# Kernel optimization log

Hardware: AMD Instinct MI355X
Metric: run time of the kernel (lower is better)

The kernel has to match this reference:

```python
import jax, jax.numpy as jnp
import numpy as np

N_NODES = 50000
N_EDGES = 800000
DIM = 64
N_ETYPES = 4
N_STEPS = 5


def setup_inputs() -> dict:
    key = jax.random.key(0)
    ks = jax.random.split(key, 10)
    feat = jax.random.normal(ks[0], (N_NODES, DIM), dtype=jnp.float32)
    src = jax.random.randint(ks[1], (N_EDGES,), 0, N_NODES, dtype=jnp.int32)
    dst = jax.random.randint(ks[2], (N_EDGES,), 0, N_NODES, dtype=jnp.int32)
    etypes = jax.random.randint(ks[3], (N_EDGES,), 0, N_ETYPES, dtype=jnp.int32)
    # per-edge-type Linear weights, xavier_normal with relu gain, zero bias
    gain = float(np.sqrt(2.0))
    std = gain * float(np.sqrt(2.0 / (DIM + DIM)))
    W = jax.random.normal(ks[4], (N_ETYPES, DIM, DIM), dtype=jnp.float32) * std  # [T, out, in]
    b = jnp.zeros((N_ETYPES, DIM), dtype=jnp.float32)
    # GRUCell params (torch layout: [3*dim, dim], gates order r,z,n), uniform(-1/sqrt(dim), 1/sqrt(dim))
    bound = 1.0 / float(np.sqrt(DIM))
    w_ih = jax.random.uniform(ks[5], (3 * DIM, DIM), minval=-bound, maxval=bound, dtype=jnp.float32)
    w_hh = jax.random.uniform(ks[6], (3 * DIM, DIM), minval=-bound, maxval=bound, dtype=jnp.float32)
    b_ih = jax.random.uniform(ks[7], (3 * DIM,), minval=-bound, maxval=bound, dtype=jnp.float32)
    b_hh = jax.random.uniform(ks[8], (3 * DIM,), minval=-bound, maxval=bound, dtype=jnp.float32)
    return {"feat": feat, "W": W, "b": b, "w_ih": w_ih, "w_hh": w_hh,
            "b_ih": b_ih, "b_hh": b_hh, "src": src, "dst": dst, "etypes": etypes}


def _gru_cell(a, h, w_ih, w_hh, b_ih, b_hh):
    gi = a @ w_ih.T + b_ih  # [N, 3*D]
    gh = h @ w_hh.T + b_hh
    i_r, i_z, i_n = jnp.split(gi, 3, axis=-1)
    h_r, h_z, h_n = jnp.split(gh, 3, axis=-1)
    r = jax.nn.sigmoid(i_r + h_r)
    z = jax.nn.sigmoid(i_z + h_z)
    n = jnp.tanh(i_n + r * h_n)
    return (1.0 - z) * n + z * h


def reference(feat, W, b, w_ih, w_hh, b_ih, b_hh, src, dst, etypes):
    n_nodes = feat.shape[0]
    h = feat
    for _ in range(N_STEPS):
        # apply every etype linear to all nodes: [N, T, D]
        h_all = jnp.einsum('nd,ted->nte', h, W) + b
        # per-edge message selects src node under its edge type: [E, D]
        m = h_all[src, etypes]
        # scatter-sum to destination nodes: [N, D]
        a = jax.ops.segment_sum(m, dst, num_segments=n_nodes)
        h = _gru_cell(a, h, w_ih, w_hh, b_ih, b_hh)
    return h
```

## Files before the change

### kernel.cpp

```cpp
#include <hip/hip_runtime.h>
#include <hip/hip_bf16.h>
#include <cstdint>

#define DIM 64
#define TD 256
#define NSTEPS 5
#define HS  68
#define GLDH 194
#define MAXDEG 64

typedef __attribute__((ext_vector_type(8))) short short8v;
typedef __attribute__((ext_vector_type(4))) float f32x4;
typedef __attribute__((ext_vector_type(8))) _Float16 half8v;

__device__ __forceinline__ float sigmoidf_(float x){ return 1.0f/(1.0f+expf(-x)); }

__device__ __forceinline__ unsigned short f2bf(float x){
  unsigned u = __builtin_bit_cast(unsigned, x);
  return (unsigned short)((u + 0x7FFFu + ((u>>16)&1u)) >> 16);
}
__device__ __forceinline__ float bf2f(unsigned short b){
  unsigned u = ((unsigned)b)<<16;
  return __builtin_bit_cast(float, u);
}

__device__ __forceinline__ void splitbf8(const float* __restrict__ p,
                                         short8v& hi, short8v& lo){
  float4 x0 = *(const float4*)p;
  float4 x1 = *(const float4*)(p+4);
  float xs[8] = {x0.x,x0.y,x0.z,x0.w,x1.x,x1.y,x1.z,x1.w};
#pragma unroll
  for(int i=0;i<8;i++){
    unsigned short hb = f2bf(xs[i]);
    float rem = xs[i] - bf2f(hb);
    hi[i] = (short)hb;
    lo[i] = (short)f2bf(rem);
  }
}

__global__ __launch_bounds__(256) void k_pack(const float* __restrict__ src,
    short* __restrict__ ph, short* __restrict__ pl, int ncoltiles, int mode){
  int idx = blockIdx.x*256 + threadIdx.x;
  int total = ncoltiles*1024;
  if (idx >= total) return;
  int e = idx & 7, lane = (idx>>3)&63, kc = (idx>>9)&1, ct = idx>>10;
  int col = ct*16 + (lane&15);
  int k = kc*32 + (lane>>4)*8 + e;
  float v;
  if (mode==0){ int t = col>>6, eo = col&63; v = src[(size_t)(t*64+eo)*64 + k]; }
  else        { v = src[(size_t)col*64 + k]; }
  unsigned short hb = f2bf(v);
  float rem = v - bf2f(hb);
  ph[idx] = (short)hb;
  pl[idx] = (short)f2bf(rem);
}

__global__ __launch_bounds__(256) void k_transform_mfma(
    const float* __restrict__ h, const short* __restrict__ pth,
    const short* __restrict__ ptl, const float* __restrict__ b,
    _Float16* __restrict__ h_all, int n_nodes){
  const int wave = threadIdx.x >> 6, lane = threadIdx.x & 63;
  const int n0 = blockIdx.x * 16;
  if (n0 >= n_nodes) return;
  const int arow = n0 + (lane & 15);
  const int kb = (lane >> 4) * 8;
  short8v ah0,al0,ah1,al1;
  splitbf8(h + (size_t)arow*DIM + kb,      ah0, al0);
  splitbf8(h + (size_t)arow*DIM + 32 + kb, ah1, al1);
  const int crow = n0 + (lane >> 4) * 4;
  const int cc = lane & 15;
#pragma unroll
  for (int i = 0; i < 4; ++i){
    int ct = wave*4 + i;
    const short8v bh0 = *(const short8v*)(pth + ((size_t)(ct*2+0)*64 + lane)*8);
    const short8v bh1 = *(const short8v*)(pth + ((size_t)(ct*2+1)*64 + lane)*8);
    const short8v bl0 = *(const short8v*)(ptl + ((size_t)(ct*2+0)*64 + lane)*8);
    const short8v bl1 = *(const short8v*)(ptl + ((size_t)(ct*2+1)*64 + lane)*8);
    float bias = b[ct*16 + cc];
    f32x4 acc = {bias,bias,bias,bias};
    acc = __builtin_amdgcn_mfma_f32_16x16x32_bf16(ah0, bh0, acc, 0,0,0);
    acc = __builtin_amdgcn_mfma_f32_16x16x32_bf16(ah1, bh1, acc, 0,0,0);
    acc = __builtin_amdgcn_mfma_f32_16x16x32_bf16(al0, bh0, acc, 0,0,0);
    acc = __builtin_amdgcn_mfma_f32_16x16x32_bf16(al1, bh1, acc, 0,0,0);
    acc = __builtin_amdgcn_mfma_f32_16x16x32_bf16(ah0, bl0, acc, 0,0,0);
    acc = __builtin_amdgcn_mfma_f32_16x16x32_bf16(ah1, bl1, acc, 0,0,0);
#pragma unroll
    for (int q=0;q<4;q++)
      h_all[(size_t)(crow + q)*TD + ct*16 + cc] = (_Float16)acc[q];
  }
}

__global__ __launch_bounds__(256) void k_scatter_ell(
    const int* __restrict__ src, const int* __restrict__ dst,
    const int* __restrict__ et, int* __restrict__ deg,
    int* __restrict__ ell, int n_edges) {
  int e = blockIdx.x * 256 + threadIdx.x;
  if (e >= n_edges) return;
  int d0 = dst[e];
  int rank = atomicAdd(&deg[d0], 1);
  if (rank < MAXDEG)
    ell[(size_t)d0 * MAXDEG + rank] = (src[e] << 2) | et[e];
}

__global__ __launch_bounds__(256) void k_step(
    const _Float16* __restrict__ h_in, _Float16* __restrict__ h_out,
    const int* __restrict__ ell, const int* __restrict__ deg,
    float* __restrict__ h,
    const short* __restrict__ pih_h, const short* __restrict__ pih_l,
    const short* __restrict__ phh_h, const short* __restrict__ phh_l,
    const float* __restrict__ b_ih, const float* __restrict__ b_hh,
    const short* __restrict__ pth, const short* __restrict__ ptl,
    const float* __restrict__ bb,
    int n_nodes, int do_transform){
  __shared__ __align__(16) char smem[4352 + 12416];
  float (*atile)[HS]      = (float(*)[HS])smem;
  float (*hnew)[HS]       = (float(*)[HS])smem;
  int   (*ells)[MAXDEG]   = (int(*)[MAXDEG])(smem + 4352);
  _Float16* gbuf          = (_Float16*)(smem + 4352);

  const int tid = threadIdx.x;
  const int wave = tid >> 6, lane = tid & 63;
  const int n0 = blockIdx.x * 16;
  if (n0 >= n_nodes) return;

  {
    int j = tid >> 4, c4 = (tid & 15) * 4;
    int4 v = *(const int4*)(ell + (size_t)(n0 + j) * MAXDEG + c4);
    *(int4*)&ells[j][c4] = v;
  }
  __syncthreads();

  {
    int j = tid >> 4;
    int q = tid & 15;
    int eslot = q >> 3;
    int dimg = q & 7;
    int node = n0 + j;
    int dg = min(deg[node], MAXDEG);
    float acc[8] = {0,0,0,0,0,0,0,0};
    int i = eslot;
    for (; i + 6 < dg; i += 8) {
      int p0 = ells[j][i], p1 = ells[j][i+2], p2 = ells[j][i+4], p3 = ells[j][i+6];
      half8v v0 = *(const half8v*)(h_in + (size_t)(p0>>2)*TD + (p0&3)*DIM + dimg*8);
      half8v v1 = *(const half8v*)(h_in + (size_t)(p1>>2)*TD + (p1&3)*DIM + dimg*8);
      half8v v2 = *(const half8v*)(h_in + (size_t)(p2>>2)*TD + (p2&3)*DIM + dimg*8);
      half8v v3 = *(const half8v*)(h_in + (size_t)(p3>>2)*TD + (p3&3)*DIM + dimg*8);
#pragma unroll
      for (int k=0;k<8;k++)
        acc[k] += ((float)v0[k] + (float)v1[k]) + ((float)v2[k] + (float)v3[k]);
    }
    for (; i < dg; i += 2) {
      int p0 = ells[j][i];
      half8v v0 = *(const half8v*)(h_in + (size_t)(p0>>2)*TD + (p0&3)*DIM + dimg*8);
#pragma unroll
      for (int k=0;k<8;k++) acc[k] += (float)v0[k];
    }
#pragma unroll
    for (int k=0;k<8;k++) acc[k] += __shfl_xor(acc[k], 8);
    if (eslot == 0) {
#pragma unroll
      for (int k=0;k<8;k++) atile[j][dimg*8+k] = acc[k];
    }
  }
  __syncthreads();

  const bool is_h = wave >= 2;
  const short* __restrict__ pbh = is_h ? phh_h : pih_h;
  const short* __restrict__ pbl = is_h ? phh_l : pih_l;
  const float* __restrict__ bv  = is_h ? b_hh : b_ih;
  _Float16* outb = gbuf + (is_h ? 16*GLDH : 0);

  const int kb = (lane >> 4) * 8;
  short8v ah0,al0,ah1,al1;
  if (is_h) {
    const float* xp = h + (size_t)(n0 + (lane & 15))*DIM;
    splitbf8(xp + kb,      ah0, al0);
    splitbf8(xp + 32 + kb, ah1, al1);
  } else {
    const float* xp = &atile[lane & 15][0];
    splitbf8(xp + kb,      ah0, al0);
    splitbf8(xp + 32 + kb, ah1, al1);
  }

  const int ct0 = (wave & 1) * 6;
  const int rr = (lane >> 4) * 4;
  const int cc = lane & 15;
#pragma unroll
  for (int i = 0; i < 6; ++i){
    int ct = ct0 + i;
    const short8v bh0 = *(const short8v*)(pbh + ((size_t)(ct*2+0)*64 + lane)*8);
    const short8v bh1 = *(const short8v*)(pbh + ((size_t)(ct*2+1)*64 + lane)*8);
    const short8v bl0 = *(const short8v*)(pbl + ((size_t)(ct*2+0)*64 + lane)*8);
    const short8v bl1 = *(const short8v*)(pbl + ((size_t)(ct*2+1)*64 + lane)*8);
    float bias = bv[ct*16 + cc];
    f32x4 acc = {bias,bias,bias,bias};
    acc = __builtin_amdgcn_mfma_f32_16x16x32_bf16(ah0, bh0, acc, 0,0,0);
    acc = __builtin_amdgcn_mfma_f32_16x16x32_bf16(ah1, bh1, acc, 0,0,0);
    acc = __builtin_amdgcn_mfma_f32_16x16x32_bf16(al0, bh0, acc, 0,0,0);
    acc = __builtin_amdgcn_mfma_f32_16x16x32_bf16(al1, bh1, acc, 0,0,0);
    acc = __builtin_amdgcn_mfma_f32_16x16x32_bf16(ah0, bl0, acc, 0,0,0);
    acc = __builtin_amdgcn_mfma_f32_16x16x32_bf16(ah1, bl1, acc, 0,0,0);
#pragma unroll
    for (int q=0;q<4;q++)
      outb[(rr+q)*GLDH + ct*16 + cc] = (_Float16)acc[q];
  }
  __syncthreads();

#pragma unroll
  for (int it=0; it<4; ++it){
    int t = it*256 + tid;
    int j = t >> 6, d = t & 63;
    float gir = (float)gbuf[j*GLDH + d];
    float giz = (float)gbuf[j*GLDH + 64 + d];
    float gin = (float)gbuf[j*GLDH + 128 + d];
    float ghr = (float)gbuf[16*GLDH + j*GLDH + d];
    float ghz = (float)gbuf[16*GLDH + j*GLDH + 64 + d];
    float ghn = (float)gbuf[16*GLDH + j*GLDH + 128 + d];
    float r  = sigmoidf_(gir + ghr);
    float z  = sigmoidf_(giz + ghz);
    float nv = tanhf    (gin + r*ghn);
    size_t off = (size_t)(n0+j)*DIM + d;
    float ho = h[off];
    float hn = (1.0f - z)*nv + z*ho;
    h[off] = hn;
    hnew[j][d] = hn;
  }
  if (!do_transform) return;
  __syncthreads();

  short8v th0,tl0,th1,tl1;
  splitbf8(&hnew[lane & 15][kb],      th0, tl0);
  splitbf8(&hnew[lane & 15][32 + kb], th1, tl1);
  const int crow = n0 + (lane >> 4) * 4;
#pragma unroll
  for (int i = 0; i < 4; ++i){
    int ct = wave*4 + i;
    const short8v bh0 = *(const short8v*)(pth + ((size_t)(ct*2+0)*64 + lane)*8);
    const short8v bh1 = *(const short8v*)(pth + ((size_t)(ct*2+1)*64 + lane)*8);
    const short8v bl0 = *(const short8v*)(ptl + ((size_t)(ct*2+0)*64 + lane)*8);
    const short8v bl1 = *(const short8v*)(ptl + ((size_t)(ct*2+1)*64 + lane)*8);
    float bias = bb[ct*16 + cc];
    f32x4 acc = {bias,bias,bias,bias};
    acc = __builtin_amdgcn_mfma_f32_16x16x32_bf16(th0, bh0, acc, 0,0,0);
    acc = __builtin_amdgcn_mfma_f32_16x16x32_bf16(th1, bh1, acc, 0,0,0);
    acc = __builtin_amdgcn_mfma_f32_16x16x32_bf16(tl0, bh0, acc, 0,0,0);
    acc = __builtin_amdgcn_mfma_f32_16x16x32_bf16(tl1, bh1, acc, 0,0,0);
    acc = __builtin_amdgcn_mfma_f32_16x16x32_bf16(th0, bl0, acc, 0,0,0);
    acc = __builtin_amdgcn_mfma_f32_16x16x32_bf16(th1, bl1, acc, 0,0,0);
#pragma unroll
    for (int q=0;q<4;q++)
      h_out[(size_t)(crow + q)*TD + ct*16 + cc] = (_Float16)acc[q];
  }
}

extern "C" void kernel_launch(void* const* d_in, const int* in_sizes, int n_in,
                              void* d_out, int out_size, void* d_ws, size_t ws_size,
                              hipStream_t stream) {
  const float* feat = (const float*)d_in[0];
  const float* W    = (const float*)d_in[1];
  const float* b    = (const float*)d_in[2];
  const float* w_ih = (const float*)d_in[3];
  const float* w_hh = (const float*)d_in[4];
  const float* b_ih = (const float*)d_in[5];
  const float* b_hh = (const float*)d_in[6];
  const int* src = (const int*)d_in[7];
  const int* dst = (const int*)d_in[8];
  const int* et  = (const int*)d_in[9];

  const int n_nodes = in_sizes[0] / DIM;
  const int n_edges = in_sizes[7];

  float* h = (float*)d_out;
  char* ws = (char*)d_ws;
  _Float16* hall0 = (_Float16*)ws;  ws += (size_t)n_nodes * TD * sizeof(_Float16);
  _Float16* hall1 = (_Float16*)ws;  ws += (size_t)n_nodes * TD * sizeof(_Float16);
  int* ell     = (int*)ws;      ws += (size_t)n_nodes * MAXDEG * sizeof(int);
  int* deg     = (int*)ws;      ws += (size_t)n_nodes * sizeof(int);
  short* pt_h  = (short*)ws;    ws += 16384 * sizeof(short);
  short* pt_l  = (short*)ws;    ws += 16384 * sizeof(short);
  short* pih_h = (short*)ws;    ws += 12288 * sizeof(short);
  short* pih_l = (short*)ws;    ws += 12288 * sizeof(short);
  short* phh_h = (short*)ws;    ws += 12288 * sizeof(short);
  short* phh_l = (short*)ws;    ws += 12288 * sizeof(short);

  hipMemcpyAsync(h, feat, (size_t)n_nodes * DIM * sizeof(float),
                 hipMemcpyDeviceToDevice, stream);

  k_pack<<<64, 256, 0, stream>>>(W,    pt_h,  pt_l,  16, 0);
  k_pack<<<48, 256, 0, stream>>>(w_ih, pih_h, pih_l, 12, 1);
  k_pack<<<48, 256, 0, stream>>>(w_hh, phh_h, phh_l, 12, 1);

  const int nblk_edges = (n_edges + 255) / 256;
  hipMemsetAsync(deg, 0, (size_t)n_nodes * sizeof(int), stream);
  k_scatter_ell<<<nblk_edges, 256, 0, stream>>>(src, dst, et, deg, ell, n_edges);

  const int rtiles = (n_nodes + 15) / 16;

  k_transform_mfma<<<rtiles, 256, 0, stream>>>(h, pt_h, pt_l, b, hall0, n_nodes);
  for (int s = 0; s < NSTEPS; ++s) {
    const _Float16* hin = (s & 1) ? hall1 : hall0;
    _Float16* hout      = (s & 1) ? hall0 : hall1;
    k_step<<<rtiles, 256, 0, stream>>>(hin, hout, ell, deg, h,
                                       pih_h, pih_l, phh_h, phh_l, b_ih, b_hh,
                                       pt_h, pt_l, b, n_nodes,
                                       (s < NSTEPS - 1) ? 1 : 0);
  }
}
```

Baseline: 308.8 us.

## Aggregate raw features per (dst,etype) then apply edge-type linear after scatter

Replaces the transform-then-gather scheme with gather-then-transform. Edges are bucketed by (destination, edge type) into a virtual ELL, raw fp16 node features (64 wide instead of 256) are summed per bucket, and a K=288 MFMA applies all four type weights plus degree-scaled bias in one pass. This cuts the gathered bytes per edge by four and removes the separate transform kernel and 256-wide intermediate buffer. In exchange there is a larger per-block MFMA, a bigger ELL (4x32 slots per node, with a tighter cap per type), and fp16 rounding of h before aggregation.

```diff
diff --git a/kernel.cpp b/kernel.cpp
--- a/kernel.cpp
+++ b/kernel.cpp
@@ -3,11 +3,11 @@
 #include <cstdint>
 
 #define DIM 64
-#define TD 256
 #define NSTEPS 5
 #define HS  68
 #define GLDH 194
-#define MAXDEG 64
+#define ATS 292
+#define MAXVDEG 32
 
 typedef __attribute__((ext_vector_type(8))) short short8v;
 typedef __attribute__((ext_vector_type(4))) float f32x4;
@@ -39,84 +39,69 @@
 }
 
 __global__ __launch_bounds__(256) void k_pack(const float* __restrict__ src,
-    short* __restrict__ ph, short* __restrict__ pl, int ncoltiles, int mode){
+    short* __restrict__ ph, short* __restrict__ pl, int ncoltiles){
   int idx = blockIdx.x*256 + threadIdx.x;
   int total = ncoltiles*1024;
   if (idx >= total) return;
   int e = idx & 7, lane = (idx>>3)&63, kc = (idx>>9)&1, ct = idx>>10;
   int col = ct*16 + (lane&15);
   int k = kc*32 + (lane>>4)*8 + e;
-  float v;
-  if (mode==0){ int t = col>>6, eo = col&63; v = src[(size_t)(t*64+eo)*64 + k]; }
-  else        { v = src[(size_t)col*64 + k]; }
+  float v = src[(size_t)col*DIM + k];
   unsigned short hb = f2bf(v);
-  float rem = v - bf2f(hb);
   ph[idx] = (short)hb;
-  pl[idx] = (short)f2bf(rem);
-}
-
-__global__ __launch_bounds__(256) void k_transform_mfma(
-    const float* __restrict__ h, const short* __restrict__ pth,
-    const short* __restrict__ ptl, const float* __restrict__ b,
-    _Float16* __restrict__ h_all, int n_nodes){
-  const int wave = threadIdx.x >> 6, lane = threadIdx.x & 63;
-  const int n0 = blockIdx.x * 16;
-  if (n0 >= n_nodes) return;
-  const int arow = n0 + (lane & 15);
-  const int kb = (lane >> 4) * 8;
-  short8v ah0,al0,ah1,al1;
-  splitbf8(h + (size_t)arow*DIM + kb,      ah0, al0);
-  splitbf8(h + (size_t)arow*DIM + 32 + kb, ah1, al1);
-  const int crow = n0 + (lane >> 4) * 4;
-  const int cc = lane & 15;
-#pragma unroll
-  for (int i = 0; i < 4; ++i){
-    int ct = wave*4 + i;
-    const short8v bh0 = *(const short8v*)(pth + ((size_t)(ct*2+0)*64 + lane)*8);
-    const short8v bh1 = *(const short8v*)(pth + ((size_t)(ct*2+1)*64 + lane)*8);
-    const short8v bl0 = *(const short8v*)(ptl + ((size_t)(ct*2+0)*64 + lane)*8);
-    const short8v bl1 = *(const short8v*)(ptl + ((size_t)(ct*2+1)*64 + lane)*8);
-    float bias = b[ct*16 + cc];
-    f32x4 acc = {bias,bias,bias,bias};
-    acc = __builtin_amdgcn_mfma_f32_16x16x32_bf16(ah0, bh0, acc, 0,0,0);
-    acc = __builtin_amdgcn_mfma_f32_16x16x32_bf16(ah1, bh1, acc, 0,0,0);
-    acc = __builtin_amdgcn_mfma_f32_16x16x32_bf16(al0, bh0, acc, 0,0,0);
-    acc = __builtin_amdgcn_mfma_f32_16x16x32_bf16(al1, bh1, acc, 0,0,0);
-    acc = __builtin_amdgcn_mfma_f32_16x16x32_bf16(ah0, bl0, acc, 0,0,0);
-    acc = __builtin_amdgcn_mfma_f32_16x16x32_bf16(ah1, bl1, acc, 0,0,0);
-#pragma unroll
-    for (int q=0;q<4;q++)
-      h_all[(size_t)(crow + q)*TD + ct*16 + cc] = (_Float16)acc[q];
-  }
-}
-
-__global__ __launch_bounds__(256) void k_scatter_ell(
+  pl[idx] = (short)f2bf(v - bf2f(hb));
+}
+
+__global__ __launch_bounds__(256) void k_pack256(const float* __restrict__ W,
+    const float* __restrict__ b, short* __restrict__ ph, short* __restrict__ pl){
+  int idx = blockIdx.x*256 + threadIdx.x;
+  if (idx >= 4*9*512) return;
+  int e = idx & 7, lane = (idx>>3)&63, r = idx>>9;
+  int kc = r % 9, ct = r / 9;
+  int col = ct*16 + (lane&15);
+  int k = kc*32 + (lane>>4)*8 + e;
+  float v = 0.0f;
+  if (k < 256){ int t = k>>6, d = k&63; v = W[(size_t)(t*64+col)*DIM + d]; }
+  else if (k < 260){ v = b[(size_t)(k-256)*DIM + col]; }
+  unsigned short hb = f2bf(v);
+  ph[idx] = (short)hb;
+  pl[idx] = (short)f2bf(v - bf2f(hb));
+}
+
+__global__ __launch_bounds__(256) void k_cast(const float* __restrict__ x,
+                                              _Float16* __restrict__ y, int n4){
+  int i = blockIdx.x*256 + threadIdx.x;
+  if (i >= n4) return;
+  float4 v = *(const float4*)(x + (size_t)i*4);
+  y[(size_t)i*4+0] = (_Float16)v.x; y[(size_t)i*4+1] = (_Float16)v.y;
+  y[(size_t)i*4+2] = (_Float16)v.z; y[(size_t)i*4+3] = (_Float16)v.w;
+}
+
+__global__ __launch_bounds__(256) void k_scatter_vell(
     const int* __restrict__ src, const int* __restrict__ dst,
-    const int* __restrict__ et, int* __restrict__ deg,
+    const int* __restrict__ et, int* __restrict__ deg4,
     int* __restrict__ ell, int n_edges) {
   int e = blockIdx.x * 256 + threadIdx.x;
   if (e >= n_edges) return;
-  int d0 = dst[e];
-  int rank = atomicAdd(&deg[d0], 1);
-  if (rank < MAXDEG)
-    ell[(size_t)d0 * MAXDEG + rank] = (src[e] << 2) | et[e];
+  int vn = dst[e]*4 + et[e];
+  int rank = atomicAdd(&deg4[vn], 1);
+  if (rank < MAXVDEG)
+    ell[(size_t)vn * MAXVDEG + rank] = src[e];
 }
 
 __global__ __launch_bounds__(256) void k_step(
-    const _Float16* __restrict__ h_in, _Float16* __restrict__ h_out,
-    const int* __restrict__ ell, const int* __restrict__ deg,
+    const _Float16* __restrict__ hb_in, _Float16* __restrict__ hb_out,
+    const int* __restrict__ ell, const int* __restrict__ deg4,
     float* __restrict__ h,
+    const short* __restrict__ pw_h, const short* __restrict__ pw_l,
     const short* __restrict__ pih_h, const short* __restrict__ pih_l,
     const short* __restrict__ phh_h, const short* __restrict__ phh_l,
     const float* __restrict__ b_ih, const float* __restrict__ b_hh,
-    const short* __restrict__ pth, const short* __restrict__ ptl,
-    const float* __restrict__ bb,
-    int n_nodes, int do_transform){
-  __shared__ __align__(16) char smem[4352 + 12416];
-  float (*atile)[HS]      = (float(*)[HS])smem;
-  float (*hnew)[HS]       = (float(*)[HS])smem;
-  int   (*ells)[MAXDEG]   = (int(*)[MAXDEG])(smem + 4352);
-  _Float16* gbuf          = (_Float16*)(smem + 4352);
+    int n_nodes, int write_hb){
+  __shared__ __align__(16) char smem[16*ATS*4 + 16*HS*4];
+  float (*atile)[ATS] = (float(*)[ATS])smem;
+  _Float16* gbuf      = (_Float16*)smem;
+  float (*abuf)[HS]   = (float(*)[HS])(smem + 16*ATS*4);
 
   const int tid = threadIdx.x;
   const int wave = tid >> 6, lane = tid & 63;
@@ -124,43 +109,66 @@
   if (n0 >= n_nodes) return;
 
   {
-    int j = tid >> 4, c4 = (tid & 15) * 4;
-    int4 v = *(const int4*)(ell + (size_t)(n0 + j) * MAXDEG + c4);
-    *(int4*)&ells[j][c4] = v;
+    int vl = tid >> 2;
+    int q  = tid & 3;
+    int jn = vl >> 2;
+    int t  = vl & 3;
+    int vng = (n0 << 2) + vl;
+    int dg = min(deg4[vng], MAXVDEG);
+    const int* ebase = ell + (size_t)vng * MAXVDEG;
+    float acc[16];
+#pragma unroll
+    for (int k=0;k<16;k++) acc[k]=0.0f;
+    int i = 0;
+    for (; i + 1 < dg; i += 2) {
+      int s0 = ebase[i], s1 = ebase[i+1];
+      half8v a0 = *(const half8v*)(hb_in + (size_t)s0*DIM + q*16);
+      half8v a1 = *(const half8v*)(hb_in + (size_t)s0*DIM + q*16 + 8);
+      half8v c0 = *(const half8v*)(hb_in + (size_t)s1*DIM + q*16);
+      half8v c1 = *(const half8v*)(hb_in + (size_t)s1*DIM + q*16 + 8);
+#pragma unroll
+      for (int k=0;k<8;k++){ acc[k]   += (float)a0[k] + (float)c0[k];
+                             acc[8+k] += (float)a1[k] + (float)c1[k]; }
+    }
+    if (i < dg) {
+      int s0 = ebase[i];
+      half8v a0 = *(const half8v*)(hb_in + (size_t)s0*DIM + q*16);
+      half8v a1 = *(const half8v*)(hb_in + (size_t)s0*DIM + q*16 + 8);
+#pragma unroll
+      for (int k=0;k<8;k++){ acc[k] += (float)a0[k]; acc[8+k] += (float)a1[k]; }
+    }
+    float* dstp = &atile[jn][t*64 + q*16];
+#pragma unroll
+    for (int w=0;w<4;w++){
+      float4 v = {acc[w*4+0],acc[w*4+1],acc[w*4+2],acc[w*4+3]};
+      *(float4*)(dstp + w*4) = v;
+    }
+    if (q == 0) atile[jn][256 + t] = (float)dg;
+    int zr = tid >> 4, zc = 260 + (tid & 15);
+    atile[zr][zc] = 0.0f;
+    atile[zr][zc + 16] = 0.0f;
   }
   __syncthreads();
 
+  const int rr = (lane >> 4) * 4;
+  const int cc = lane & 15;
   {
-    int j = tid >> 4;
-    int q = tid & 15;
-    int eslot = q >> 3;
-    int dimg = q & 7;
-    int node = n0 + j;
-    int dg = min(deg[node], MAXDEG);
-    float acc[8] = {0,0,0,0,0,0,0,0};
-    int i = eslot;
-    for (; i + 6 < dg; i += 8) {
-      int p0 = ells[j][i], p1 = ells[j][i+2], p2 = ells[j][i+4], p3 = ells[j][i+6];
-      half8v v0 = *(const half8v*)(h_in + (size_t)(p0>>2)*TD + (p0&3)*DIM + dimg*8);
-      half8v v1 = *(const half8v*)(h_in + (size_t)(p1>>2)*TD + (p1&3)*DIM + dimg*8);
-      half8v v2 = *(const half8v*)(h_in + (size_t)(p2>>2)*TD + (p2&3)*DIM + dimg*8);
-      half8v v3 = *(const half8v*)(h_in + (size_t)(p3>>2)*TD + (p3&3)*DIM + dimg*8);
-#pragma unroll
-      for (int k=0;k<8;k++)
-        acc[k] += ((float)v0[k] + (float)v1[k]) + ((float)v2[k] + (float)v3[k]);
-    }
-    for (; i < dg; i += 2) {
-      int p0 = ells[j][i];
-      half8v v0 = *(const half8v*)(h_in + (size_t)(p0>>2)*TD + (p0&3)*DIM + dimg*8);
-#pragma unroll
-      for (int k=0;k<8;k++) acc[k] += (float)v0[k];
-    }
-#pragma unroll
-    for (int k=0;k<8;k++) acc[k] += __shfl_xor(acc[k], 8);
-    if (eslot == 0) {
-#pragma unroll
-      for (int k=0;k<8;k++) atile[j][dimg*8+k] = acc[k];
-    }
+    const float* arow = &atile[lane & 15][0];
+    const int koff = (lane >> 4) * 8;
+    f32x4 acc4 = {0.f,0.f,0.f,0.f};
+#pragma unroll
+    for (int kc = 0; kc < 9; ++kc){
+      short8v ah, al;
+      splitbf8(arow + kc*32 + koff, ah, al);
+      const short8v bh = *(const short8v*)(pw_h + ((size_t)(wave*9+kc)*64 + lane)*8);
+      const short8v bl = *(const short8v*)(pw_l + ((size_t)(wave*9+kc)*64 + lane)*8);
+      acc4 = __builtin_amdgcn_mfma_f32_16x16x32_bf16(ah, bl, acc4, 0,0,0);
+      acc4 = __builtin_amdgcn_mfma_f32_16x16x32_bf16(al, bh, acc4, 0,0,0);
+      acc4 = __builtin_amdgcn_mfma_f32_16x16x32_bf16(ah, bh, acc4, 0,0,0);
+    }
+    __syncthreads();
+#pragma unroll
+    for (int q=0;q<4;q++) abuf[rr+q][wave*16 + cc] = acc4[q];
   }
   __syncthreads();
 
@@ -177,14 +185,12 @@
     splitbf8(xp + kb,      ah0, al0);
     splitbf8(xp + 32 + kb, ah1, al1);
   } else {
-    const float* xp = &atile[lane & 15][0];
+    const float* xp = &abuf[lane & 15][0];
     splitbf8(xp + kb,      ah0, al0);
     splitbf8(xp + 32 + kb, ah1, al1);
   }
 
   const int ct0 = (wave & 1) * 6;
-  const int rr = (lane >> 4) * 4;
-  const int cc = lane & 15;
 #pragma unroll
   for (int i = 0; i < 6; ++i){
     int ct = ct0 + i;
@@ -223,33 +229,7 @@
     float ho = h[off];
     float hn = (1.0f - z)*nv + z*ho;
     h[off] = hn;
-    hnew[j][d] = hn;
-  }
-  if (!do_transform) return;
-  __syncthreads();
-
-  short8v th0,tl0,th1,tl1;
-  splitbf8(&hnew[lane & 15][kb],      th0, tl0);
-  splitbf8(&hnew[lane & 15][32 + kb], th1, tl1);
-  const int crow = n0 + (lane >> 4) * 4;
-#pragma unroll
-  for (int i = 0; i < 4; ++i){
-    int ct = wave*4 + i;
-    const short8v bh0 = *(const short8v*)(pth + ((size_t)(ct*2+0)*64 + lane)*8);
-    const short8v bh1 = *(const short8v*)(pth + ((size_t)(ct*2+1)*64 + lane)*8);
-    const short8v bl0 = *(const short8v*)(ptl + ((size_t)(ct*2+0)*64 + lane)*8);
-    const short8v bl1 = *(const short8v*)(ptl + ((size_t)(ct*2+1)*64 + lane)*8);
-    float bias = bb[ct*16 + cc];
-    f32x4 acc = {bias,bias,bias,bias};
-    acc = __builtin_amdgcn_mfma_f32_16x16x32_bf16(th0, bh0, acc, 0,0,0);
-    acc = __builtin_amdgcn_mfma_f32_16x16x32_bf16(th1, bh1, acc, 0,0,0);
-    acc = __builtin_amdgcn_mfma_f32_16x16x32_bf16(tl0, bh0, acc, 0,0,0);
-    acc = __builtin_amdgcn_mfma_f32_16x16x32_bf16(tl1, bh1, acc, 0,0,0);
-    acc = __builtin_amdgcn_mfma_f32_16x16x32_bf16(th0, bl0, acc, 0,0,0);
-    acc = __builtin_amdgcn_mfma_f32_16x16x32_bf16(th1, bl1, acc, 0,0,0);
-#pragma unroll
-    for (int q=0;q<4;q++)
-      h_out[(size_t)(crow + q)*TD + ct*16 + cc] = (_Float16)acc[q];
+    if (write_hb) hb_out[off] = (_Float16)hn;
   }
 }
 
@@ -272,37 +252,37 @@
 
   float* h = (float*)d_out;
   char* ws = (char*)d_ws;
-  _Float16* hall0 = (_Float16*)ws;  ws += (size_t)n_nodes * TD * sizeof(_Float16);
-  _Float16* hall1 = (_Float16*)ws;  ws += (size_t)n_nodes * TD * sizeof(_Float16);
-  int* ell     = (int*)ws;      ws += (size_t)n_nodes * MAXDEG * sizeof(int);
-  int* deg     = (int*)ws;      ws += (size_t)n_nodes * sizeof(int);
-  short* pt_h  = (short*)ws;    ws += 16384 * sizeof(short);
-  short* pt_l  = (short*)ws;    ws += 16384 * sizeof(short);
-  short* pih_h = (short*)ws;    ws += 12288 * sizeof(short);
-  short* pih_l = (short*)ws;    ws += 12288 * sizeof(short);
-  short* phh_h = (short*)ws;    ws += 12288 * sizeof(short);
-  short* phh_l = (short*)ws;    ws += 12288 * sizeof(short);
+  _Float16* hb0 = (_Float16*)ws;  ws += (size_t)n_nodes * DIM * sizeof(_Float16);
+  _Float16* hb1 = (_Float16*)ws;  ws += (size_t)n_nodes * DIM * sizeof(_Float16);
+  int* ell  = (int*)ws;   ws += (size_t)n_nodes * 4 * MAXVDEG * sizeof(int);
+  int* deg4 = (int*)ws;   ws += (size_t)n_nodes * 4 * sizeof(int);
+  short* pw_h  = (short*)ws;  ws += 18432 * sizeof(short);
+  short* pw_l  = (short*)ws;  ws += 18432 * sizeof(short);
+  short* pih_h = (short*)ws;  ws += 12288 * sizeof(short);
+  short* pih_l = (short*)ws;  ws += 12288 * sizeof(short);
+  short* phh_h = (short*)ws;  ws += 12288 * sizeof(short);
+  short* phh_l = (short*)ws;  ws += 12288 * sizeof(short);
 
   hipMemcpyAsync(h, feat, (size_t)n_nodes * DIM * sizeof(float),
                  hipMemcpyDeviceToDevice, stream);
 
-  k_pack<<<64, 256, 0, stream>>>(W,    pt_h,  pt_l,  16, 0);
-  k_pack<<<48, 256, 0, stream>>>(w_ih, pih_h, pih_l, 12, 1);
-  k_pack<<<48, 256, 0, stream>>>(w_hh, phh_h, phh_l, 12, 1);
+  k_pack256<<<72, 256, 0, stream>>>(W, b, pw_h, pw_l);
+  k_pack<<<48, 256, 0, stream>>>(w_ih, pih_h, pih_l, 12);
+  k_pack<<<48, 256, 0, stream>>>(w_hh, phh_h, phh_l, 12);
+  k_cast<<<(n_nodes*DIM/4 + 255)/256, 256, 0, stream>>>(feat, hb0, n_nodes*DIM/4);
 
   const int nblk_edges = (n_edges + 255) / 256;
-  hipMemsetAsync(deg, 0, (size_t)n_nodes * sizeof(int), stream);
-  k_scatter_ell<<<nblk_edges, 256, 0, stream>>>(src, dst, et, deg, ell, n_edges);
+  hipMemsetAsync(deg4, 0, (size_t)n_nodes * 4 * sizeof(int), stream);
+  k_scatter_vell<<<nblk_edges, 256, 0, stream>>>(src, dst, et, deg4, ell, n_edges);
 
   const int rtiles = (n_nodes + 15) / 16;
 
-  k_transform_mfma<<<rtiles, 256, 0, stream>>>(h, pt_h, pt_l, b, hall0, n_nodes);
   for (int s = 0; s < NSTEPS; ++s) {
-    const _Float16* hin = (s & 1) ? hall1 : hall0;
-    _Float16* hout      = (s & 1) ? hall0 : hall1;
-    k_step<<<rtiles, 256, 0, stream>>>(hin, hout, ell, deg, h,
-                                       pih_h, pih_l, phh_h, phh_l, b_ih, b_hh,
-                                       pt_h, pt_l, b, n_nodes,
+    const _Float16* hin = (s & 1) ? hb1 : hb0;
+    _Float16* hout      = (s & 1) ? hb0 : hb1;
+    k_step<<<rtiles, 256, 0, stream>>>(hin, hout, ell, deg4, h,
+                                       pw_h, pw_l, pih_h, pih_l, phh_h, phh_l,
+                                       b_ih, b_hh, n_nodes,
                                        (s < NSTEPS - 1) ? 1 : 0);
   }
 }
```

Measured after the change: 323.6 us. 1.05x slower.

## Overlap hidden-state GEMM with neighbor gather via wave specialization

Applied to the files above, without the earlier changes.

Waves 0-1 now gather and sum neighbor messages, one node per 8 threads, reading ELL indices directly from global memory with int4 loads. Meanwhile waves 2-3 compute the h·W_hh gate GEMM. After a barrier all four waves split the a·W_ih GEMM. This removes the staging of ELL indices in shared memory, one barrier and the cross-lane shuffle, and overlaps the gather latency with MFMA work. In exchange only half the block performs the memory-bound gather, so fewer loads are in flight per node group.

```diff
diff --git a/kernel.cpp b/kernel.cpp
--- a/kernel.cpp
+++ b/kernel.cpp
@@ -113,96 +113,115 @@
     const float* __restrict__ bb,
     int n_nodes, int do_transform){
   __shared__ __align__(16) char smem[4352 + 12416];
-  float (*atile)[HS]      = (float(*)[HS])smem;
-  float (*hnew)[HS]       = (float(*)[HS])smem;
-  int   (*ells)[MAXDEG]   = (int(*)[MAXDEG])(smem + 4352);
-  _Float16* gbuf          = (_Float16*)(smem + 4352);
+  float (*atile)[HS] = (float(*)[HS])smem;
+  float (*hnew)[HS]  = (float(*)[HS])smem;
+  _Float16* gbuf     = (_Float16*)(smem + 4352);
 
   const int tid = threadIdx.x;
   const int wave = tid >> 6, lane = tid & 63;
   const int n0 = blockIdx.x * 16;
   if (n0 >= n_nodes) return;
 
-  {
-    int j = tid >> 4, c4 = (tid & 15) * 4;
-    int4 v = *(const int4*)(ell + (size_t)(n0 + j) * MAXDEG + c4);
-    *(int4*)&ells[j][c4] = v;
-  }
-  __syncthreads();
-
-  {
-    int j = tid >> 4;
-    int q = tid & 15;
-    int eslot = q >> 3;
-    int dimg = q & 7;
+  const int kb = (lane >> 4) * 8;
+  const int rr = (lane >> 4) * 4;
+  const int cc = lane & 15;
+
+  if (wave < 2) {
+    int j = tid >> 3, q = tid & 7;
     int node = n0 + j;
     int dg = min(deg[node], MAXDEG);
+    const int* eb = ell + (size_t)node * MAXDEG;
     float acc[8] = {0,0,0,0,0,0,0,0};
-    int i = eslot;
-    for (; i + 6 < dg; i += 8) {
-      int p0 = ells[j][i], p1 = ells[j][i+2], p2 = ells[j][i+4], p3 = ells[j][i+6];
-      half8v v0 = *(const half8v*)(h_in + (size_t)(p0>>2)*TD + (p0&3)*DIM + dimg*8);
-      half8v v1 = *(const half8v*)(h_in + (size_t)(p1>>2)*TD + (p1&3)*DIM + dimg*8);
-      half8v v2 = *(const half8v*)(h_in + (size_t)(p2>>2)*TD + (p2&3)*DIM + dimg*8);
-      half8v v3 = *(const half8v*)(h_in + (size_t)(p3>>2)*TD + (p3&3)*DIM + dimg*8);
+    int i = 0;
+    for (; i + 7 < dg; i += 8) {
+      int4 pa = *(const int4*)(eb + i);
+      int4 pb = *(const int4*)(eb + i + 4);
+      half8v v0 = *(const half8v*)(h_in + (size_t)(pa.x>>2)*TD + (pa.x&3)*DIM + q*8);
+      half8v v1 = *(const half8v*)(h_in + (size_t)(pa.y>>2)*TD + (pa.y&3)*DIM + q*8);
+      half8v v2 = *(const half8v*)(h_in + (size_t)(pa.z>>2)*TD + (pa.z&3)*DIM + q*8);
+      half8v v3 = *(const half8v*)(h_in + (size_t)(pa.w>>2)*TD + (pa.w&3)*DIM + q*8);
+      half8v v4 = *(const half8v*)(h_in + (size_t)(pb.x>>2)*TD + (pb.x&3)*DIM + q*8);
+      half8v v5 = *(const half8v*)(h_in + (size_t)(pb.y>>2)*TD + (pb.y&3)*DIM + q*8);
+      half8v v6 = *(const half8v*)(h_in + (size_t)(pb.z>>2)*TD + (pb.z&3)*DIM + q*8);
+      half8v v7 = *(const half8v*)(h_in + (size_t)(pb.w>>2)*TD + (pb.w&3)*DIM + q*8);
+#pragma unroll
+      for (int k=0;k<8;k++)
+        acc[k] += (((float)v0[k] + (float)v1[k]) + ((float)v2[k] + (float)v3[k]))
+                + (((float)v4[k] + (float)v5[k]) + ((float)v6[k] + (float)v7[k]));
+    }
+    for (; i + 3 < dg; i += 4) {
+      int4 pa = *(const int4*)(eb + i);
+      half8v v0 = *(const half8v*)(h_in + (size_t)(pa.x>>2)*TD + (pa.x&3)*DIM + q*8);
+      half8v v1 = *(const half8v*)(h_in + (size_t)(pa.y>>2)*TD + (pa.y&3)*DIM + q*8);
+      half8v v2 = *(const half8v*)(h_in + (size_t)(pa.z>>2)*TD + (pa.z&3)*DIM + q*8);
+      half8v v3 = *(const half8v*)(h_in + (size_t)(pa.w>>2)*TD + (pa.w&3)*DIM + q*8);
 #pragma unroll
       for (int k=0;k<8;k++)
         acc[k] += ((float)v0[k] + (float)v1[k]) + ((float)v2[k] + (float)v3[k]);
     }
-    for (; i < dg; i += 2) {
-      int p0 = ells[j][i];
-      half8v v0 = *(const half8v*)(h_in + (size_t)(p0>>2)*TD + (p0&3)*DIM + dimg*8);
+    for (; i < dg; ++i) {
+      int p0 = eb[i];
+      half8v v0 = *(const half8v*)(h_in + (size_t)(p0>>2)*TD + (p0&3)*DIM + q*8);
 #pragma unroll
       for (int k=0;k<8;k++) acc[k] += (float)v0[k];
     }
-#pragma unroll
-    for (int k=0;k<8;k++) acc[k] += __shfl_xor(acc[k], 8);
-    if (eslot == 0) {
-#pragma unroll
-      for (int k=0;k<8;k++) atile[j][dimg*8+k] = acc[k];
-    }
-  }
-  __syncthreads();
-
-  const bool is_h = wave >= 2;
-  const short* __restrict__ pbh = is_h ? phh_h : pih_h;
-  const short* __restrict__ pbl = is_h ? phh_l : pih_l;
-  const float* __restrict__ bv  = is_h ? b_hh : b_ih;
-  _Float16* outb = gbuf + (is_h ? 16*GLDH : 0);
-
-  const int kb = (lane >> 4) * 8;
-  short8v ah0,al0,ah1,al1;
-  if (is_h) {
+    float4 o0 = {acc[0],acc[1],acc[2],acc[3]};
+    float4 o1 = {acc[4],acc[5],acc[6],acc[7]};
+    *(float4*)&atile[j][q*8]     = o0;
+    *(float4*)&atile[j][q*8 + 4] = o1;
+  } else {
+    _Float16* outb = gbuf + 16*GLDH;
     const float* xp = h + (size_t)(n0 + (lane & 15))*DIM;
+    short8v ah0,al0,ah1,al1;
     splitbf8(xp + kb,      ah0, al0);
     splitbf8(xp + 32 + kb, ah1, al1);
-  } else {
+    const int ct0 = (wave & 1) * 6;
+#pragma unroll
+    for (int i = 0; i < 6; ++i){
+      int ct = ct0 + i;
+      const short8v bh0 = *(const short8v*)(phh_h + ((size_t)(ct*2+0)*64 + lane)*8);
+      const short8v bh1 = *(const short8v*)(phh_h + ((size_t)(ct*2+1)*64 + lane)*8);
+      const short8v bl0 = *(const short8v*)(phh_l + ((size_t)(ct*2+0)*64 + lane)*8);
+      const short8v bl1 = *(const short8v*)(phh_l + ((size_t)(ct*2+1)*64 + lane)*8);
+      float bias = b_hh[ct*16 + cc];
+      f32x4 acc = {bias,bias,bias,bias};
+      acc = __builtin_amdgcn_mfma_f32_16x16x32_bf16(ah0, bh0, acc, 0,0,0);
+      acc = __builtin_amdgcn_mfma_f32_16x16x32_bf16(ah1, bh1, acc, 0,0,0);
+      acc = __builtin_amdgcn_mfma_f32_16x16x32_bf16(al0, bh0, acc, 0,0,0);
+      acc = __builtin_amdgcn_mfma_f32_16x16x32_bf16(al1, bh1, acc, 0,0,0);
+      acc = __builtin_amdgcn_mfma_f32_16x16x32_bf16(ah0, bl0, acc, 0,0,0);
+      acc = __builtin_amdgcn_mfma_f32_16x16x32_bf16(ah1, bl1, acc, 0,0,0);
+#pragma unroll
+      for (int q=0;q<4;q++)
+        outb[(rr+q)*GLDH + ct*16 + cc] = (_Float16)acc[q];
+    }
+  }
+  __syncthreads();
+
+  {
     const float* xp = &atile[lane & 15][0];
+    short8v ah0,al0,ah1,al1;
     splitbf8(xp + kb,      ah0, al0);
     splitbf8(xp + 32 + kb, ah1, al1);
-  }
-
-  const int ct0 = (wave & 1) * 6;
-  const int rr = (lane >> 4) * 4;
-  const int cc = lane & 15;
-#pragma unroll
-  for (int i = 0; i < 6; ++i){
-    int ct = ct0 + i;
-    const short8v bh0 = *(const short8v*)(pbh + ((size_t)(ct*2+0)*64 + lane)*8);
-    const short8v bh1 = *(const short8v*)(pbh + ((size_t)(ct*2+1)*64 + lane)*8);
-    const short8v bl0 = *(const short8v*)(pbl + ((size_t)(ct*2+0)*64 + lane)*8);
-    const short8v bl1 = *(const short8v*)(pbl + ((size_t)(ct*2+1)*64 + lane)*8);
-    float bias = bv[ct*16 + cc];
-    f32x4 acc = {bias,bias,bias,bias};
-    acc = __builtin_amdgcn_mfma_f32_16x16x32_bf16(ah0, bh0, acc, 0,0,0);
-    acc = __builtin_amdgcn_mfma_f32_16x16x32_bf16(ah1, bh1, acc, 0,0,0);
-    acc = __builtin_amdgcn_mfma_f32_16x16x32_bf16(al0, bh0, acc, 0,0,0);
-    acc = __builtin_amdgcn_mfma_f32_16x16x32_bf16(al1, bh1, acc, 0,0,0);
-    acc = __builtin_amdgcn_mfma_f32_16x16x32_bf16(ah0, bl0, acc, 0,0,0);
-    acc = __builtin_amdgcn_mfma_f32_16x16x32_bf16(ah1, bl1, acc, 0,0,0);
-#pragma unroll
-    for (int q=0;q<4;q++)
-      outb[(rr+q)*GLDH + ct*16 + cc] = (_Float16)acc[q];
+#pragma unroll
+    for (int i = 0; i < 3; ++i){
+      int ct = wave*3 + i;
+      const short8v bh0 = *(const short8v*)(pih_h + ((size_t)(ct*2+0)*64 + lane)*8);
+      const short8v bh1 = *(const short8v*)(pih_h + ((size_t)(ct*2+1)*64 + lane)*8);
+      const short8v bl0 = *(const short8v*)(pih_l + ((size_t)(ct*2+0)*64 + lane)*8);
+      const short8v bl1 = *(const short8v*)(pih_l + ((size_t)(ct*2+1)*64 + lane)*8);
+      float bias = b_ih[ct*16 + cc];
+      f32x4 acc = {bias,bias,bias,bias};
+      acc = __builtin_amdgcn_mfma_f32_16x16x32_bf16(ah0, bh0, acc, 0,0,0);
+      acc = __builtin_amdgcn_mfma_f32_16x16x32_bf16(ah1, bh1, acc, 0,0,0);
+      acc = __builtin_amdgcn_mfma_f32_16x16x32_bf16(al0, bh0, acc, 0,0,0);
+      acc = __builtin_amdgcn_mfma_f32_16x16x32_bf16(al1, bh1, acc, 0,0,0);
+      acc = __builtin_amdgcn_mfma_f32_16x16x32_bf16(ah0, bl0, acc, 0,0,0);
+      acc = __builtin_amdgcn_mfma_f32_16x16x32_bf16(ah1, bl1, acc, 0,0,0);
+#pragma unroll
+      for (int q=0;q<4;q++)
+        gbuf[(rr+q)*GLDH + ct*16 + cc] = (_Float16)acc[q];
+    }
   }
   __syncthreads();
 
```

Measured after the change: 329.4 us. 6.6% more time.

## Balance edge gather across threads with per-block edge map and LDS atomics

Applied to the files above, without the earlier changes.

Replaces the fixed per-node gather, where 16 threads served each node and were bounded by its degree, with a block-level flattened edge list. A prefix sum over node degrees builds a map from edge slot to node, and 32 edge-slot groups each take an equal contiguous chunk of the block's edges. Partial sums are flushed to shared memory with atomics whenever the node changes. This evens out load imbalance from varying degrees, but adds the scan, an extra barrier, LDS atomics, and a dependent global load of ell per edge instead of staging ell in shared memory.

```diff
diff --git a/kernel.cpp b/kernel.cpp
--- a/kernel.cpp
+++ b/kernel.cpp
@@ -113,96 +113,117 @@
     const float* __restrict__ bb,
     int n_nodes, int do_transform){
   __shared__ __align__(16) char smem[4352 + 12416];
-  float (*atile)[HS]      = (float(*)[HS])smem;
-  float (*hnew)[HS]       = (float(*)[HS])smem;
-  int   (*ells)[MAXDEG]   = (int(*)[MAXDEG])(smem + 4352);
-  _Float16* gbuf          = (_Float16*)(smem + 4352);
+  float (*atile)[HS] = (float(*)[HS])smem;
+  float (*hnew)[HS]  = (float(*)[HS])smem;
+  int*            cum  = (int*)(smem + 4352);
+  unsigned short* map  = (unsigned short*)(smem + 4352 + 68);
+  _Float16* gbuf       = (_Float16*)(smem + 4352);
 
   const int tid = threadIdx.x;
   const int wave = tid >> 6, lane = tid & 63;
   const int n0 = blockIdx.x * 16;
   if (n0 >= n_nodes) return;
 
-  {
-    int j = tid >> 4, c4 = (tid & 15) * 4;
-    int4 v = *(const int4*)(ell + (size_t)(n0 + j) * MAXDEG + c4);
-    *(int4*)&ells[j][c4] = v;
-  }
+  if (wave == 0) {
+    int d = (lane < 16) ? min(deg[n0 + lane], MAXDEG) : 0;
+    int s = d;
+#pragma unroll
+    for (int off = 1; off < 16; off <<= 1) {
+      int t = __shfl_up(s, off);
+      if (lane >= off && lane < 16) s += t;
+    }
+    if (lane < 16) cum[lane + 1] = s;
+    if (lane == 0) cum[0] = 0;
+  }
+  for (int t = tid; t < 16*HS; t += 256) ((float*)atile)[t] = 0.0f;
   __syncthreads();
 
   {
     int j = tid >> 4;
-    int q = tid & 15;
-    int eslot = q >> 3;
-    int dimg = q & 7;
-    int node = n0 + j;
-    int dg = min(deg[node], MAXDEG);
-    float acc[8] = {0,0,0,0,0,0,0,0};
-    int i = eslot;
-    for (; i + 6 < dg; i += 8) {
-      int p0 = ells[j][i], p1 = ells[j][i+2], p2 = ells[j][i+4], p3 = ells[j][i+6];
-      half8v v0 = *(const half8v*)(h_in + (size_t)(p0>>2)*TD + (p0&3)*DIM + dimg*8);
-      half8v v1 = *(const half8v*)(h_in + (size_t)(p1>>2)*TD + (p1&3)*DIM + dimg*8);
-      half8v v2 = *(const half8v*)(h_in + (size_t)(p2>>2)*TD + (p2&3)*DIM + dimg*8);
-      half8v v3 = *(const half8v*)(h_in + (size_t)(p3>>2)*TD + (p3&3)*DIM + dimg*8);
-#pragma unroll
-      for (int k=0;k<8;k++)
-        acc[k] += ((float)v0[k] + (float)v1[k]) + ((float)v2[k] + (float)v3[k]);
-    }
-    for (; i < dg; i += 2) {
-      int p0 = ells[j][i];
-      half8v v0 = *(const half8v*)(h_in + (size_t)(p0>>2)*TD + (p0&3)*DIM + dimg*8);
-#pragma unroll
-      for (int k=0;k<8;k++) acc[k] += (float)v0[k];
-    }
-#pragma unroll
-    for (int k=0;k<8;k++) acc[k] += __shfl_xor(acc[k], 8);
-    if (eslot == 0) {
-#pragma unroll
-      for (int k=0;k<8;k++) atile[j][dimg*8+k] = acc[k];
-    }
-  }
-  __syncthreads();
-
-  const bool is_h = wave >= 2;
-  const short* __restrict__ pbh = is_h ? phh_h : pih_h;
-  const short* __restrict__ pbl = is_h ? phh_l : pih_l;
-  const float* __restrict__ bv  = is_h ? b_hh : b_ih;
-  _Float16* outb = gbuf + (is_h ? 16*GLDH : 0);
+    int base = cum[j];
+    int dj = cum[j + 1] - base;
+    for (int r = tid & 15; r < dj; r += 16)
+      map[base + r] = (unsigned short)((j << 6) | r);
+  }
+  __syncthreads();
+
+  {
+    const int Eb = cum[16];
+    const int nch = (Eb + 31) >> 5;
+    const int es = tid >> 3, q = tid & 7;
+    int w0 = es * nch;
+    int w1 = min(w0 + nch, Eb);
+    float acc[8];
+    int jcur = -1;
+    for (int w = w0; w < w1; ++w) {
+      int m = map[w];
+      int j = m >> 6, r = m & 63;
+      int p = ell[(size_t)(n0 + j) * MAXDEG + r];
+      half8v v = *(const half8v*)(h_in + (size_t)(p >> 2) * TD + (p & 3) * DIM + q * 8);
+      if (j != jcur) {
+        if (jcur >= 0) {
+          float* ap = &atile[jcur][q * 8];
+#pragma unroll
+          for (int k = 0; k < 8; ++k) atomicAdd(&ap[k], acc[k]);
+        }
+        jcur = j;
+#pragma unroll
+        for (int k = 0; k < 8; ++k) acc[k] = (float)v[k];
+      } else {
+#pragma unroll
+        for (int k = 0; k < 8; ++k) acc[k] += (float)v[k];
+      }
+    }
+    if (jcur >= 0) {
+      float* ap = &atile[jcur][q * 8];
+#pragma unroll
+      for (int k = 0; k < 8; ++k) atomicAdd(&ap[k], acc[k]);
+    }
+  }
+  __syncthreads();
 
   const int kb = (lane >> 4) * 8;
-  short8v ah0,al0,ah1,al1;
-  if (is_h) {
-    const float* xp = h + (size_t)(n0 + (lane & 15))*DIM;
-    splitbf8(xp + kb,      ah0, al0);
-    splitbf8(xp + 32 + kb, ah1, al1);
-  } else {
-    const float* xp = &atile[lane & 15][0];
-    splitbf8(xp + kb,      ah0, al0);
-    splitbf8(xp + 32 + kb, ah1, al1);
-  }
-
-  const int ct0 = (wave & 1) * 6;
   const int rr = (lane >> 4) * 4;
   const int cc = lane & 15;
-#pragma unroll
-  for (int i = 0; i < 6; ++i){
-    int ct = ct0 + i;
-    const short8v bh0 = *(const short8v*)(pbh + ((size_t)(ct*2+0)*64 + lane)*8);
-    const short8v bh1 = *(const short8v*)(pbh + ((size_t)(ct*2+1)*64 + lane)*8);
-    const short8v bl0 = *(const short8v*)(pbl + ((size_t)(ct*2+0)*64 + lane)*8);
-    const short8v bl1 = *(const short8v*)(pbl + ((size_t)(ct*2+1)*64 + lane)*8);
-    float bias = bv[ct*16 + cc];
-    f32x4 acc = {bias,bias,bias,bias};
-    acc = __builtin_amdgcn_mfma_f32_16x16x32_bf16(ah0, bh0, acc, 0,0,0);
-    acc = __builtin_amdgcn_mfma_f32_16x16x32_bf16(ah1, bh1, acc, 0,0,0);
-    acc = __builtin_amdgcn_mfma_f32_16x16x32_bf16(al0, bh0, acc, 0,0,0);
-    acc = __builtin_amdgcn_mfma_f32_16x16x32_bf16(al1, bh1, acc, 0,0,0);
-    acc = __builtin_amdgcn_mfma_f32_16x16x32_bf16(ah0, bl0, acc, 0,0,0);
-    acc = __builtin_amdgcn_mfma_f32_16x16x32_bf16(ah1, bl1, acc, 0,0,0);
-#pragma unroll
-    for (int q=0;q<4;q++)
-      outb[(rr+q)*GLDH + ct*16 + cc] = (_Float16)acc[q];
+
+  {
+    const bool is_h = wave >= 2;
+    const short* __restrict__ pbh = is_h ? phh_h : pih_h;
+    const short* __restrict__ pbl = is_h ? phh_l : pih_l;
+    const float* __restrict__ bv  = is_h ? b_hh : b_ih;
+    _Float16* outb = gbuf + (is_h ? 16*GLDH : 0);
+
+    short8v ah0,al0,ah1,al1;
+    if (is_h) {
+      const float* xp = h + (size_t)(n0 + (lane & 15))*DIM;
+      splitbf8(xp + kb,      ah0, al0);
+      splitbf8(xp + 32 + kb, ah1, al1);
+    } else {
+      const float* xp = &atile[lane & 15][0];
+      splitbf8(xp + kb,      ah0, al0);
+      splitbf8(xp + 32 + kb, ah1, al1);
+    }
+    __syncthreads();
+    const int ct0 = (wave & 1) * 6;
+#pragma unroll
+    for (int i = 0; i < 6; ++i){
+      int ct = ct0 + i;
+      const short8v bh0 = *(const short8v*)(pbh + ((size_t)(ct*2+0)*64 + lane)*8);
+      const short8v bh1 = *(const short8v*)(pbh + ((size_t)(ct*2+1)*64 + lane)*8);
+      const short8v bl0 = *(const short8v*)(pbl + ((size_t)(ct*2+0)*64 + lane)*8);
+      const short8v bl1 = *(const short8v*)(pbl + ((size_t)(ct*2+1)*64 + lane)*8);
+      float bias = bv[ct*16 + cc];
+      f32x4 acc = {bias,bias,bias,bias};
+      acc = __builtin_amdgcn_mfma_f32_16x16x32_bf16(ah0, bh0, acc, 0,0,0);
+      acc = __builtin_amdgcn_mfma_f32_16x16x32_bf16(ah1, bh1, acc, 0,0,0);
+      acc = __builtin_amdgcn_mfma_f32_16x16x32_bf16(al0, bh0, acc, 0,0,0);
+      acc = __builtin_amdgcn_mfma_f32_16x16x32_bf16(al1, bh1, acc, 0,0,0);
+      acc = __builtin_amdgcn_mfma_f32_16x16x32_bf16(ah0, bl0, acc, 0,0,0);
+      acc = __builtin_amdgcn_mfma_f32_16x16x32_bf16(ah1, bl1, acc, 0,0,0);
+#pragma unroll
+      for (int q=0;q<4;q++)
+        outb[(rr+q)*GLDH + ct*16 + cc] = (_Float16)acc[q];
+    }
   }
   __syncthreads();
 
```

Result: slower. 482.3 us (+56.2%).
